# Kernel optimization log

Hardware: AMD Instinct MI355X
Metric: run time of the kernel (lower is better)

Reference implementation:

```python
import jax, jax.numpy as jnp
import numpy as np

HEADS = 16
D_HEAD = 64
EPS = 1e-5


def _ln(x, g, b):
    m = jnp.mean(x, axis=-1, keepdims=True)
    v = jnp.var(x, axis=-1, keepdims=True)
    return (x - m) * jax.lax.rsqrt(v + EPS) * g + b


def _attn(xq, xc, Wq, Wk, Wv, Wo, bo):
    # Wq: [dim, inner], Wk/Wv: [ctx_dim, inner], Wo: [inner, dim]
    B, N, _ = xq.shape
    S = xc.shape[1]
    q = (xq @ Wq).reshape(B, N, HEADS, D_HEAD)
    k = (xc @ Wk).reshape(B, S, HEADS, D_HEAD)
    v = (xc @ Wv).reshape(B, S, HEADS, D_HEAD)
    scale = D_HEAD ** -0.5
    scores = jnp.einsum('bnhd,bshd->bhns', q, k) * scale
    attn = jax.nn.softmax(scores, axis=-1)
    out = jnp.einsum('bhns,bshd->bnhd', attn, v).reshape(B, N, HEADS * D_HEAD)
    return out @ Wo + bo


def _geglu_ff(x, Wp, bp, Wf, bf):
    h = x @ Wp + bp  # [B,N,2*inner]
    a, gate = jnp.split(h, 2, axis=-1)
    # torch F.gelu default is exact (erf) gelu
    return (a * jax.nn.gelu(gate, approximate=False)) @ Wf + bf


def setup_inputs() -> dict:
    key = jax.random.key(0)
    ks = jax.random.split(key, 16)
    dim, ctx, inner, ffin = 1024, 768, HEADS * D_HEAD, 4 * 1024
    def w(k, i, o):
        return jax.random.normal(k, (i, o), jnp.float32) * (i ** -0.5)
    inp = {
        'x': jax.random.normal(ks[0], (4, 2048, dim), jnp.float32),
        'context': jax.random.normal(ks[1], (4, 77, ctx), jnp.float32),
        'Wq1': w(ks[2], dim, inner), 'Wk1': w(ks[3], dim, inner), 'Wv1': w(ks[4], dim, inner),
        'Wo1': w(ks[5], inner, dim), 'bo1': jnp.zeros((dim,), jnp.float32),
        'Wq2': w(ks[6], dim, inner), 'Wk2': w(ks[7], ctx, inner), 'Wv2': w(ks[8], ctx, inner),
        'Wo2': w(ks[9], inner, dim), 'bo2': jnp.zeros((dim,), jnp.float32),
        'Wp': w(ks[10], dim, 2 * ffin), 'bp': jnp.zeros((2 * ffin,), jnp.float32),
        'Wf': w(ks[11], ffin, dim), 'bf': jnp.zeros((dim,), jnp.float32),
        'g1': jnp.ones((dim,), jnp.float32), 'b1': jnp.zeros((dim,), jnp.float32),
        'g2': jnp.ones((dim,), jnp.float32), 'b2': jnp.zeros((dim,), jnp.float32),
        'g3': jnp.ones((dim,), jnp.float32), 'b3': jnp.zeros((dim,), jnp.float32),
    }
    return inp


def reference(x, context, Wq1, Wk1, Wv1, Wo1, bo1, Wq2, Wk2, Wv2, Wo2, bo2,
              Wp, bp, Wf, bf, g1, b1, g2, b2, g3, b3):
    x = _attn(_ln(x, g1, b1), _ln(x, g1, b1), Wq1, Wk1, Wv1, Wo1, bo1) + x
    x = _attn(_ln(x, g2, b2), context, Wq2, Wk2, Wv2, Wo2, bo2) + x
    x = _geglu_ff(_ln(x, g3, b3), Wp, bp, Wf, bf) + x
    return x
```

## Files before the change

### kernel.cpp

```cpp
#include <hip/hip_runtime.h>

typedef unsigned short u16;
typedef __bf16 bf16x8 __attribute__((ext_vector_type(8)));
typedef float f32x4 __attribute__((ext_vector_type(4)));

#define HEADS 16
#define DHEAD 64
#define DIM 1024
#define NTOK 2048
#define BATCH 4
#define CTXD 768
#define SCROSS 77
#define FFIN 4096

__device__ inline float bf2f(u16 v) { return __uint_as_float(((unsigned)v) << 16); }
__device__ inline u16 f2bf(float f) {
    unsigned u = __float_as_uint(f);
    unsigned r = u + 0x7fffu + ((u >> 16) & 1u);
    return (u16)(r >> 16);
}
__device__ inline f32x4 f4zero() { f32x4 v; v[0]=0.f; v[1]=0.f; v[2]=0.f; v[3]=0.f; return v; }
__device__ inline bf16x8 as_bf16x8(uint4 u) { union { uint4 a; bf16x8 b; } c; c.a = u; return c.b; }

__device__ inline void gload_lds16(const u16* g, u16* l) {
    __builtin_amdgcn_global_load_lds((const __attribute__((address_space(1))) unsigned*)g,
                                     (__attribute__((address_space(3))) unsigned*)l, 16, 0, 0);
}

__global__ __launch_bounds__(256) void wt_k(const float* __restrict__ W, u16* __restrict__ WT,
                                            int K, int N, float scale, int remap) {
    __shared__ u16 Ts[64][72];
    int k0 = blockIdx.x * 64, n0 = blockIdx.y * 64;
    int t = threadIdx.x;
    int r = t >> 2, c4 = (t & 3) * 16;
    const float* wp = W + (size_t)(k0 + r) * N + n0 + c4;
    #pragma unroll
    for (int j = 0; j < 4; j++) {
        float4 v = *(const float4*)(wp + j * 4);
        Ts[c4 + j * 4 + 0][r] = f2bf(v.x * scale);
        Ts[c4 + j * 4 + 1][r] = f2bf(v.y * scale);
        Ts[c4 + j * 4 + 2][r] = f2bf(v.z * scale);
        Ts[c4 + j * 4 + 3][r] = f2bf(v.w * scale);
    }
    __syncthreads();
    int n = t >> 2, kc = (t & 3) * 16;
    int ng = n0 + n;
    if (remap) ng = ((ng & 4095) >> 4) * 32 + ((ng >> 12) << 4) + (ng & 15);
    u16* op = WT + (size_t)ng * K + k0 + kc;
    *(uint4*)op       = *(const uint4*)&Ts[n][kc];
    *(uint4*)(op + 8) = *(const uint4*)&Ts[n][kc + 8];
}

__global__ __launch_bounds__(256) void cvt_k(const float* __restrict__ X, u16* __restrict__ Y, int n4) {
    int i = blockIdx.x * 256 + threadIdx.x;
    if (i < n4) {
        float4 v = *(const float4*)(X + (size_t)i * 4);
        uint2 o;
        o.x = (unsigned)f2bf(v.x) | ((unsigned)f2bf(v.y) << 16);
        o.y = (unsigned)f2bf(v.z) | ((unsigned)f2bf(v.w) << 16);
        *(uint2*)(Y + (size_t)i * 4) = o;
    }
}

__global__ __launch_bounds__(256) void ln_k(const float* __restrict__ X, const float* __restrict__ G,
                                            const float* __restrict__ Bt, u16* __restrict__ Y) {
    int row = blockIdx.x;
    int t = threadIdx.x;
    int w = t >> 6, lane = t & 63;
    float4 xv = *(const float4*)(X + (size_t)row * DIM + t * 4);
    float s = xv.x + xv.y + xv.z + xv.w;
    float s2 = xv.x*xv.x + xv.y*xv.y + xv.z*xv.z + xv.w*xv.w;
    for (int off = 1; off < 64; off <<= 1) {
        s  += __shfl_xor(s,  off, 64);
        s2 += __shfl_xor(s2, off, 64);
    }
    __shared__ float rs[4], rs2[4];
    if (lane == 0) { rs[w] = s; rs2[w] = s2; }
    __syncthreads();
    float S_ = rs[0] + rs[1] + rs[2] + rs[3];
    float S2_ = rs2[0] + rs2[1] + rs2[2] + rs2[3];
    float mean = S_ * (1.0f / DIM);
    float var = fmaxf(S2_ * (1.0f / DIM) - mean * mean, 0.f);
    float rstd = rsqrtf(var + 1e-5f);
    int col = t * 4;
    float4 g = *(const float4*)(G + col);
    float4 b = *(const float4*)(Bt + col);
    float y0 = (xv.x - mean) * rstd * g.x + b.x;
    float y1 = (xv.y - mean) * rstd * g.y + b.y;
    float y2 = (xv.z - mean) * rstd * g.z + b.z;
    float y3 = (xv.w - mean) * rstd * g.w + b.w;
    uint2 o;
    o.x = (unsigned)f2bf(y0) | ((unsigned)f2bf(y1) << 16);
    o.y = (unsigned)f2bf(y2) | ((unsigned)f2bf(y3) << 16);
    *(uint2*)(Y + (size_t)row * DIM + col) = o;
}

template<typename TC, bool RESID>
__global__ __launch_bounds__(256) void gemm128(const u16* __restrict__ A, int lda,
                                               const u16* __restrict__ BT,
                                               const float* __restrict__ bias, const float* resid,
                                               TC* C, int ldc, int M, int N, int K) {
    __shared__ __align__(16) u16 As[128 * 32];
    __shared__ __align__(16) u16 Bs[128 * 32];
    int m0 = blockIdx.x * 128, n0 = blockIdx.y * 128;
    int t = threadIdx.x;
    int w = t >> 6, lane = t & 63;
    int quad = lane >> 4, l16 = lane & 15;
    int mh = (w & 1) * 64, nh = (w >> 1) * 64;
    f32x4 acc[4][4];
    #pragma unroll
    for (int i = 0; i < 4; i++)
        #pragma unroll
        for (int j = 0; j < 4; j++) acc[i][j] = f4zero();
    int sr = t >> 2;
    int sc8 = (((t & 3) ^ ((sr >> 1) & 3)) * 8);
    int ra0 = min(m0 + sr, M - 1);
    int ra1 = min(m0 + sr + 64, M - 1);
    const u16* ga0 = A + (size_t)ra0 * lda + sc8;
    const u16* ga1 = A + (size_t)ra1 * lda + sc8;
    const u16* gb0 = BT + (size_t)(n0 + sr) * K + sc8;
    const u16* gb1 = BT + (size_t)(n0 + sr + 64) * K + sc8;
    u16* lA0 = &As[w * 512];
    u16* lA1 = &As[2048 + w * 512];
    u16* lB0 = &Bs[w * 512];
    u16* lB1 = &Bs[2048 + w * 512];
    int rq = ((quad ^ ((l16 >> 1) & 3)) * 8);
    for (int k0 = 0; k0 < K; k0 += 32) {
        __syncthreads();
        gload_lds16(ga0 + k0, lA0);
        gload_lds16(ga1 + k0, lA1);
        gload_lds16(gb0 + k0, lB0);
        gload_lds16(gb1 + k0, lB1);
        __syncthreads();
        bf16x8 af[4], bfv[4];
        #pragma unroll
        for (int i = 0; i < 4; i++) {
            af[i]  = as_bf16x8(*(const uint4*)&As[(mh + i * 16 + l16) * 32 + rq]);
            bfv[i] = as_bf16x8(*(const uint4*)&Bs[(nh + i * 16 + l16) * 32 + rq]);
        }
        #pragma unroll
        for (int i = 0; i < 4; i++)
            #pragma unroll
            for (int j = 0; j < 4; j++)
                acc[i][j] = __builtin_amdgcn_mfma_f32_16x16x32_bf16(af[i], bfv[j], acc[i][j], 0, 0, 0);
    }
    #pragma unroll
    for (int j = 0; j < 4; j++) {
        int gn = n0 + nh + j * 16 + l16;
        float bv = bias ? bias[gn] : 0.f;
        #pragma unroll
        for (int i = 0; i < 4; i++) {
            #pragma unroll
            for (int r = 0; r < 4; r++) {
                int gm = m0 + mh + i * 16 + quad * 4 + r;
                if (gm < M) {
                    float v = acc[i][j][r] + bv;
                    if constexpr (RESID) v += resid[(size_t)gm * N + gn];
                    if constexpr (__is_same(TC, u16)) C[(size_t)gm * ldc + gn] = f2bf(v);
                    else                              C[(size_t)gm * ldc + gn] = v;
                }
            }
        }
    }
}


#define BAR() __builtin_amdgcn_s_barrier()
#define SB0() __builtin_amdgcn_sched_barrier(0)
#define PRIO1() __builtin_amdgcn_s_setprio(1)
#define PRIO0() __builtin_amdgcn_s_setprio(0)
#define WAIT_VM6() asm volatile("s_waitcnt vmcnt(6)" ::: "memory")
#define WAIT_VM0() asm volatile("s_waitcnt vmcnt(0)" ::: "memory")
#define WAIT_LGKM0() asm volatile("s_waitcnt lgkmcnt(0)" ::: "memory")
#define WAIT_LGKM8() asm volatile("s_waitcnt lgkmcnt(8)" ::: "memory")

#define STAGE_A_R(P, h, q, TAU) gload_lds16(gA + (size_t)((h) * 128 + (q) * 64) * 1024 + (TAU) * 64, \
                                            lA + (P) * 16384 + (h) * 8192 + (q) * 4096)
#define STAGE_B_R(P, h, q, TAU) gload_lds16(gB + (size_t)((h) * 128 + (q) * 64) * 1024 + (TAU) * 64, \
                                            lB + (P) * 16384 + (h) * 8192 + (q) * 4096)
#define RD_A(P, fi, ks) as_bf16x8(*(const uint4*)(rdA + (P) * 32768 + (fi) * 2048 + ((ks) ? o1 : o0)))
#define RD_B(P, fj, ks) as_bf16x8(*(const uint4*)(rdB + (P) * 32768 + (fj) * 2048 + ((ks) ? o1 : o0)))
#define MM(ai, aj, av, bv) acc[ai][aj] = __builtin_amdgcn_mfma_f32_16x16x32_bf16(av, bv, acc[ai][aj], 0, 0, 0)

#define TILE256(P, S0, S1, T, LAST) do {                                              \
    if (LAST) { WAIT_VM0(); } else { WAIT_VM6(); }                                    \
    BAR(); SB0();                                                                     \
                        \
    Ar[0][0] = RD_A(P, 0, 0); Ar[0][1] = RD_A(P, 0, 1);                               \
    Ar[1][0] = RD_A(P, 1, 0); Ar[1][1] = RD_A(P, 1, 1);                               \
    Ar[2][0] = RD_A(P, 2, 0); Ar[2][1] = RD_A(P, 2, 1);                               \
    Ar[3][0] = RD_A(P, 3, 0); Ar[3][1] = RD_A(P, 3, 1);                               \
    BrA[0][0] = RD_B(P, 0, 0); BrA[0][1] = RD_B(P, 0, 1);                             \
    BrA[1][0] = RD_B(P, 1, 0); BrA[1][1] = RD_B(P, 1, 1);                             \
    if (S0) { STAGE_B_R((P) ^ 1, 1, 0, (T) + 1); STAGE_B_R((P) ^ 1, 1, 1, (T) + 1); } \
    WAIT_LGKM8();                                                                     \
    BAR(); WAIT_LGKM0(); SB0(); PRIO1();                                              \
    MM(0,0,Ar[0][0],BrA[0][0]); MM(1,0,Ar[1][0],BrA[0][0]); MM(2,0,Ar[2][0],BrA[0][0]); MM(3,0,Ar[3][0],BrA[0][0]); \
    MM(0,1,Ar[0][0],BrA[1][0]); MM(1,1,Ar[1][0],BrA[1][0]); MM(2,1,Ar[2][0],BrA[1][0]); MM(3,1,Ar[3][0],BrA[1][0]); \
    MM(0,0,Ar[0][1],BrA[0][1]); MM(1,0,Ar[1][1],BrA[0][1]); MM(2,0,Ar[2][1],BrA[0][1]); MM(3,0,Ar[3][1],BrA[0][1]); \
    MM(0,1,Ar[0][1],BrA[1][1]); MM(1,1,Ar[1][1],BrA[1][1]); MM(2,1,Ar[2][1],BrA[1][1]); MM(3,1,Ar[3][1],BrA[1][1]); \
    PRIO0(); SB0(); BAR();                                                            \
                                       \
    BrB[0][0] = RD_B(P, 2, 0); BrB[0][1] = RD_B(P, 2, 1);                             \
    BrB[1][0] = RD_B(P, 3, 0); BrB[1][1] = RD_B(P, 3, 1);                             \
    if (S1) { STAGE_A_R(P, 0, 0, (T) + 2); STAGE_A_R(P, 1, 0, (T) + 2); }             \
    BAR(); WAIT_LGKM0(); SB0(); PRIO1();                                              \
    MM(0,2,Ar[0][0],BrB[0][0]); MM(1,2,Ar[1][0],BrB[0][0]); MM(2,2,Ar[2][0],BrB[0][0]); MM(3,2,Ar[3][0],BrB[0][0]); \
    MM(0,3,Ar[0][0],BrB[1][0]); MM(1,3,Ar[1][0],BrB[1][0]); MM(2,3,Ar[2][0],BrB[1][0]); MM(3,3,Ar[3][0],BrB[1][0]); \
    MM(0,2,Ar[0][1],BrB[0][1]); MM(1,2,Ar[1][1],BrB[0][1]); MM(2,2,Ar[2][1],BrB[0][1]); MM(3,2,Ar[3][1],BrB[0][1]); \
    MM(0,3,Ar[0][1],BrB[1][1]); MM(1,3,Ar[1][1],BrB[1][1]); MM(2,3,Ar[2][1],BrB[1][1]); MM(3,3,Ar[3][1],BrB[1][1]); \
    PRIO0(); SB0(); BAR();                                                            \
      \
    Ar[0][0] = RD_A(P, 4, 0); Ar[0][1] = RD_A(P, 4, 1);                               \
    Ar[1][0] = RD_A(P, 5, 0); Ar[1][1] = RD_A(P, 5, 1);                               \
    Ar[2][0] = RD_A(P, 6, 0); Ar[2][1] = RD_A(P, 6, 1);                               \
    Ar[3][0] = RD_A(P, 7, 0); Ar[3][1] = RD_A(P, 7, 1);                               \
    if (S1) { STAGE_B_R(P, 0, 0, (T) + 2); STAGE_B_R(P, 0, 1, (T) + 2); }             \
    BAR(); WAIT_LGKM0(); SB0(); PRIO1();                                              \
    MM(4,2,Ar[0][0],BrB[0][0]); MM(5,2,Ar[1][0],BrB[0][0]); MM(6,2,Ar[2][0],BrB[0][0]); MM(7,2,Ar[3][0],BrB[0][0]); \
    MM(4,3,Ar[0][0],BrB[1][0]); MM(5,3,Ar[1][0],BrB[1][0]); MM(6,3,Ar[2][0],BrB[1][0]); MM(7,3,Ar[3][0],BrB[1][0]); \
    MM(4,2,Ar[0][1],BrB[0][1]); MM(5,2,Ar[1][1],BrB[0][1]); MM(6,2,Ar[2][1],BrB[0][1]); MM(7,2,Ar[3][1],BrB[0][1]); \
    MM(4,3,Ar[0][1],BrB[1][1]); MM(5,3,Ar[1][1],BrB[1][1]); MM(6,3,Ar[2][1],BrB[1][1]); MM(7,3,Ar[3][1],BrB[1][1]); \
    PRIO0(); SB0(); BAR();                                                            \
           \
    if (S1) { STAGE_A_R(P, 0, 1, (T) + 2); STAGE_A_R(P, 1, 1, (T) + 2); }             \
    BAR(); SB0(); PRIO1();                                                            \
    MM(4,0,Ar[0][0],BrA[0][0]); MM(5,0,Ar[1][0],BrA[0][0]); MM(6,0,Ar[2][0],BrA[0][0]); MM(7,0,Ar[3][0],BrA[0][0]); \
    MM(4,1,Ar[0][0],BrA[1][0]); MM(5,1,Ar[1][0],BrA[1][0]); MM(6,1,Ar[2][0],BrA[1][0]); MM(7,1,Ar[3][0],BrA[1][0]); \
    MM(4,0,Ar[0][1],BrA[0][1]); MM(5,0,Ar[1][1],BrA[0][1]); MM(6,0,Ar[2][1],BrA[0][1]); MM(7,0,Ar[3][1],BrA[0][1]); \
    MM(4,1,Ar[0][1],BrA[1][1]); MM(5,1,Ar[1][1],BrA[1][1]); MM(6,1,Ar[2][1],BrA[1][1]); MM(7,1,Ar[3][1],BrA[1][1]); \
    PRIO0(); SB0();                                                                   \
} while (0)

template<int NBY, int LDC, int EPI>
__global__ __launch_bounds__(512, 2) void gemm256(const u16* __restrict__ A,
                                                  const u16* __restrict__ BT,
                                                  const float* __restrict__ bias,
                                                  u16* __restrict__ C) {
    __shared__ __align__(16) u16 As[2][16384];
    __shared__ __align__(16) u16 Bs[2][16384];
    int t = threadIdx.x;
    int w = t >> 6, lane = t & 63;
    int quad = lane >> 4, l16 = lane & 15;
    int wm = w >> 2, wn = w & 3;
    int bid = blockIdx.x;
    int cpx = (int)gridDim.x >> 3;
    int swz = (bid & 7) * cpx + (bid >> 3);
    int bx = swz / NBY, by = swz % NBY;
    int m0 = bx << 8, n0 = by << 8;

    int ar = t >> 3;
    int ac = (((t & 7) ^ (ar & 7)) << 3);
    const u16* gA = A + (size_t)(m0 + ar) * 1024 + ac;
    const u16* gB = BT + (size_t)(n0 + ar) * 1024 + ac;
    u16* lA = &As[0][0] + (w << 9);
    u16* lB = &Bs[0][0] + (w << 9);
    const char* rdA = (const char*)&As[0][0] + (((wm << 7) + l16) << 7);
    const char* rdB = (const char*)&Bs[0][0] + (((wn << 6) + l16) << 7);
    int o0 = (quad << 4) ^ ((l16 & 7) << 4);
    int o1 = o0 ^ 64;

    f32x4 acc[8][4];
    #pragma unroll
    for (int i = 0; i < 8; i++)
        #pragma unroll
        for (int j = 0; j < 4; j++) acc[i][j] = f4zero();

    STAGE_A_R(0, 0, 0, 0); STAGE_A_R(0, 1, 0, 0);
    STAGE_B_R(0, 0, 0, 0); STAGE_B_R(0, 0, 1, 0);
    STAGE_A_R(0, 0, 1, 0); STAGE_A_R(0, 1, 1, 0);
    STAGE_B_R(0, 1, 0, 0); STAGE_B_R(0, 1, 1, 0);
    STAGE_A_R(1, 0, 0, 1); STAGE_A_R(1, 1, 0, 1);
    STAGE_B_R(1, 0, 0, 1); STAGE_B_R(1, 0, 1, 1);
    STAGE_A_R(1, 0, 1, 1); STAGE_A_R(1, 1, 1, 1);

    bf16x8 Ar[4][2], BrA[2][2], BrB[2][2];
    #pragma unroll 1
    for (int tt = 0; tt < 14; tt += 2) {
        TILE256(0, 1, 1, tt, 0);
        TILE256(1, 1, 1, tt + 1, 0);
    }
    TILE256(0, 1, 0, 14, 0);
    TILE256(1, 0, 0, 15, 1);

    if constexpr (EPI == 0) {
        int gm0 = m0 + wm * 128 + quad * 4;
        int gn0 = n0 + wn * 64 + l16;
        #pragma unroll
        for (int fi = 0; fi < 8; fi++)
            #pragma unroll
            for (int fj = 0; fj < 4; fj++)
                #pragma unroll
                for (int r = 0; r < 4; r++)
                    C[(size_t)(gm0 + fi * 16 + r) * LDC + gn0 + fj * 16] = f2bf(acc[fi][fj][r]);
    } else {
        int gm0 = m0 + wm * 128 + quad * 4;
        int oc0 = (n0 >> 1) + wn * 32 + l16;
        #pragma unroll
        for (int jp = 0; jp < 2; jp++) {
            int oc = oc0 + jp * 16;
            float ba = bias[oc];
            float bg = bias[FFIN + oc];
            #pragma unroll
            for (int fi = 0; fi < 8; fi++)
                #pragma unroll
                for (int r = 0; r < 4; r++) {
                    float a = acc[fi][2 * jp][r] + ba;
                    float g = acc[fi][2 * jp + 1][r] + bg;
                    float v = a * (0.5f * g * (1.f + erff(g * 0.70710678118654752f)));
                    C[(size_t)(gm0 + fi * 16 + r) * LDC + oc] = f2bf(v);
                }
        }
    }
}

__global__ __launch_bounds__(256) void attn_k(const u16* Q, int ldq, const u16* __restrict__ K,
                                              const u16* __restrict__ V, int ldkv,
                                              u16* O, int S) {
    __shared__ __align__(16) u16 Ksh[128 * 64];
    __shared__ __align__(16) u16 Vt[64 * 128];
    __shared__ __align__(16) u16 Pb[4][16 * 128];
    int bh = blockIdx.x;
    int b = bh >> 4, h = bh & 15;
    int q0 = blockIdx.y * 64;
    int t = threadIdx.x;
    int w = t >> 6, lane = t & 63;
    int quad = lane >> 4, l16 = lane & 15;
    int sw = (l16 & 7) << 3;
    const u16* Qp = Q + ((size_t)b * NTOK + q0) * ldq + h * DHEAD;
    const u16* Kp = K + (size_t)b * S * ldkv + h * DHEAD;
    const u16* Vp = V + (size_t)b * S * ldkv + h * DHEAD;
    bf16x8 qf[2];
    #pragma unroll
    for (int ds = 0; ds < 2; ds++)
        qf[ds] = as_bf16x8(*(const uint4*)(Qp + (size_t)(w * 16 + l16) * ldq + ds * 32 + quad * 8));
    float l_l = 0.f;
    f32x4 o_acc[4];
    #pragma unroll
    for (int dt = 0; dt < 4; dt++) o_acc[dt] = f4zero();
    int kr8 = lane >> 3;
    int ksl = ((lane & 7) ^ kr8) * 8;
    int vd = (t >> 5) * 8;
    int vk = (t & 31) * 4;
    int nkt = (S + 127) / 128;
    for (int kt = 0; kt < nkt; kt++) {
        int kbase = kt * 128;
        bool full = (kbase + 128) <= S;
        __syncthreads();
        #pragma unroll
        for (int i = 0; i < 4; i++) {
            int r = min(kbase + (i * 4 + w) * 8 + kr8, S - 1);
            gload_lds16(Kp + (size_t)r * ldkv + ksl, &Ksh[(i * 4 + w) * 512]);
        }
        {
            union { uint4 u; u16 e[8]; } vr[4];
            #pragma unroll
            for (int j = 0; j < 4; j++) {
                int key = min(kbase + vk + j, S - 1);
                vr[j].u = *(const uint4*)(Vp + (size_t)key * ldkv + vd);
            }
            #pragma unroll
            for (int d = 0; d < 8; d++) {
                int row = vd + d;
                uint2 p;
                p.x = (unsigned)vr[0].e[d] | ((unsigned)vr[1].e[d] << 16);
                p.y = (unsigned)vr[2].e[d] | ((unsigned)vr[3].e[d] << 16);
                *(uint2*)&Vt[row * 128 + (vk ^ ((row & 7) << 3))] = p;
            }
        }
        __syncthreads();
        f32x4 sc[8];
        PRIO1();
        #pragma unroll
        for (int sub = 0; sub < 8; sub++) {
            const u16* kr = &Ksh[(sub * 16 + l16) * 64];
            bf16x8 kf0 = as_bf16x8(*(const uint4*)(kr + ((quad * 8) ^ sw)));
            bf16x8 kf1 = as_bf16x8(*(const uint4*)(kr + ((32 + quad * 8) ^ sw)));
            f32x4 s = __builtin_amdgcn_mfma_f32_16x16x32_bf16(kf0, qf[0], f4zero(), 0, 0, 0);
            sc[sub] = __builtin_amdgcn_mfma_f32_16x16x32_bf16(kf1, qf[1], s, 0, 0, 0);
        }
        PRIO0();
        if (!full) {
            #pragma unroll
            for (int sub = 0; sub < 8; sub++)
                #pragma unroll
                for (int r = 0; r < 4; r++)
                    if (kbase + sub * 16 + quad * 4 + r >= S) sc[sub][r] = -1e30f;
        }
        float psum = 0.f;
        #pragma unroll
        for (int sub = 0; sub < 8; sub++) {
            float p0 = __builtin_amdgcn_exp2f(sc[sub][0]);
            float p1 = __builtin_amdgcn_exp2f(sc[sub][1]);
            float p2 = __builtin_amdgcn_exp2f(sc[sub][2]);
            float p3 = __builtin_amdgcn_exp2f(sc[sub][3]);
            psum += (p0 + p1) + (p2 + p3);
            uint2 pk;
            pk.x = __builtin_amdgcn_perm(__float_as_uint(p1), __float_as_uint(p0), 0x07060302);
            pk.y = __builtin_amdgcn_perm(__float_as_uint(p3), __float_as_uint(p2), 0x07060302);
            *(uint2*)&Pb[w][l16 * 128 + ((sub * 16 + quad * 4) ^ sw)] = pk;
        }
        l_l += psum;
        PRIO1();
        #pragma unroll
        for (int kk = 0; kk < 4; kk++) {
            bf16x8 pf = as_bf16x8(*(const uint4*)&Pb[w][l16 * 128 + ((kk * 32 + quad * 8) ^ sw)]);
            #pragma unroll
            for (int dt = 0; dt < 4; dt++) {
                bf16x8 vf = as_bf16x8(*(const uint4*)&Vt[(dt * 16 + l16) * 128 + ((kk * 32 + quad * 8) ^ sw)]);
                o_acc[dt] = __builtin_amdgcn_mfma_f32_16x16x32_bf16(pf, vf, o_acc[dt], 0, 0, 0);
            }
        }
        PRIO0();
    }
    float l_tot = l_l;
    l_tot += __shfl_xor(l_tot, 16, 64);
    l_tot += __shfl_xor(l_tot, 32, 64);
    #pragma unroll
    for (int r = 0; r < 4; r++) {
        float lr = __shfl(l_tot, quad * 4 + r, 64);
        float invl = (lr > 0.f) ? (1.f / lr) : 0.f;
        int gq = q0 + w * 16 + quad * 4 + r;
        #pragma unroll
        for (int dt = 0; dt < 4; dt++) {
            O[((size_t)b * NTOK + gq) * ldq + h * DHEAD + dt * 16 + l16] = f2bf(o_acc[dt][r] * invl);
        }
    }
}

extern "C" void kernel_launch(void* const* d_in, const int* in_sizes, int n_in,
                              void* d_out, int out_size, void* d_ws, size_t ws_size,
                              hipStream_t stream) {
    const float* x   = (const float*)d_in[0];
    const float* ctx = (const float*)d_in[1];
    const float* Wq1 = (const float*)d_in[2];
    const float* Wk1 = (const float*)d_in[3];
    const float* Wv1 = (const float*)d_in[4];
    const float* Wo1 = (const float*)d_in[5];
    const float* bo1 = (const float*)d_in[6];
    const float* Wq2 = (const float*)d_in[7];
    const float* Wk2 = (const float*)d_in[8];
    const float* Wv2 = (const float*)d_in[9];
    const float* Wo2 = (const float*)d_in[10];
    const float* bo2 = (const float*)d_in[11];
    const float* Wp  = (const float*)d_in[12];
    const float* bp  = (const float*)d_in[13];
    const float* Wf  = (const float*)d_in[14];
    const float* bfb = (const float*)d_in[15];
    const float* g1  = (const float*)d_in[16];
    const float* b1  = (const float*)d_in[17];
    const float* g2  = (const float*)d_in[18];
    const float* b2  = (const float*)d_in[19];
    const float* g3  = (const float*)d_in[20];
    const float* b3  = (const float*)d_in[21];
    float* out = (float*)d_out;

    const int M = BATCH * NTOK;
    const int Mc = BATCH * SCROSS;
    u16* ws = (u16*)d_ws;
    size_t o = 0;
    u16* WqT1 = ws + o; o += (size_t)DIM * DIM;
    u16* WkT1 = ws + o; o += (size_t)DIM * DIM;
    u16* WvT1 = ws + o; o += (size_t)DIM * DIM;
    u16* WoT1 = ws + o; o += (size_t)DIM * DIM;
    u16* WqT2 = ws + o; o += (size_t)DIM * DIM;
    u16* WoT2 = ws + o; o += (size_t)DIM * DIM;
    u16* WkT2 = ws + o; o += (size_t)DIM * CTXD;
    u16* WvT2 = ws + o; o += (size_t)DIM * CTXD;
    u16* WpT  = ws + o; o += (size_t)(2 * FFIN) * DIM;
    u16* WfT  = ws + o; o += (size_t)DIM * FFIN;
    u16* ctxb = ws + o; o += (size_t)Mc * CTXD;
    u16* KVc  = ws + o; o += (size_t)Mc * 2048;
    u16* P    = ws + o; o += (size_t)M * DIM;
    u16* QKV  = ws + o; o += (size_t)M * 3072;
    u16* reg2 = ws + o; o += (size_t)M * DIM * 2;
    float* X1 = (float*)reg2;
    u16* gb = QKV;

    dim3 blk(256);
    const float qscale = 0.125f * 1.4426950408889634f;

    wt_k<<<dim3(16, 16), blk, 0, stream>>>(Wq1, WqT1, DIM, DIM, qscale, 0);
    wt_k<<<dim3(16, 16), blk, 0, stream>>>(Wk1, WkT1, DIM, DIM, 1.f, 0);
    wt_k<<<dim3(16, 16), blk, 0, stream>>>(Wv1, WvT1, DIM, DIM, 1.f, 0);
    wt_k<<<dim3(16, 16), blk, 0, stream>>>(Wo1, WoT1, DIM, DIM, 1.f, 0);
    wt_k<<<dim3(16, 16), blk, 0, stream>>>(Wq2, WqT2, DIM, DIM, qscale, 0);
    wt_k<<<dim3(16, 16), blk, 0, stream>>>(Wo2, WoT2, DIM, DIM, 1.f, 0);
    wt_k<<<dim3(12, 16), blk, 0, stream>>>(Wk2, WkT2, CTXD, DIM, 1.f, 0);
    wt_k<<<dim3(12, 16), blk, 0, stream>>>(Wv2, WvT2, CTXD, DIM, 1.f, 0);
    wt_k<<<dim3(16, 128), blk, 0, stream>>>(Wp, WpT, DIM, 2 * FFIN, 1.f, 1);
    wt_k<<<dim3(64, 16), blk, 0, stream>>>(Wf, WfT, FFIN, DIM, 1.f, 0);
    cvt_k<<<dim3((Mc * CTXD / 4 + 255) / 256), blk, 0, stream>>>(ctx, ctxb, Mc * CTXD / 4);

    ln_k<<<dim3(M), blk, 0, stream>>>(x, g1, b1, P);
    gemm128<u16, false><<<dim3(M / 128, 3072 / 128), blk, 0, stream>>>(
        P, DIM, WqT1, nullptr, nullptr, QKV, 3072, M, 3072, DIM);
    attn_k<<<dim3(BATCH * HEADS, NTOK / 64), blk, 0, stream>>>(
        QKV, 3072, QKV + 1024, QKV + 2048, 3072, QKV, NTOK);
    gemm128<float, true><<<dim3(M / 128, DIM / 128), blk, 0, stream>>>(
        QKV, 3072, WoT1, bo1, x, X1, DIM, M, DIM, DIM);

    ln_k<<<dim3(M), blk, 0, stream>>>(X1, g2, b2, P);
    gemm128<u16, false><<<dim3(M / 128, DIM / 128), blk, 0, stream>>>(
        P, DIM, WqT2, nullptr, nullptr, QKV, 3072, M, DIM, DIM);
    gemm128<u16, false><<<dim3((Mc + 127) / 128, 2048 / 128), blk, 0, stream>>>(
        ctxb, CTXD, WkT2, nullptr, nullptr, KVc, 2048, Mc, 2048, CTXD);
    attn_k<<<dim3(BATCH * HEADS, NTOK / 64), blk, 0, stream>>>(
        QKV, 3072, KVc, KVc + 1024, 2048, QKV, SCROSS);
    gemm128<float, true><<<dim3(M / 128, DIM / 128), blk, 0, stream>>>(
        QKV, 3072, WoT2, bo2, X1, out, DIM, M, DIM, DIM);

    ln_k<<<dim3(M), blk, 0, stream>>>(out, g3, b3, P);
    gemm256<32, 4096, 1><<<dim3(32 * 32), dim3(512), 0, stream>>>(P, WpT, bp, gb);
    gemm128<float, true><<<dim3(M / 128, DIM / 128), blk, 0, stream>>>(
        gb, FFIN, WfT, bfb, out, out, DIM, M, DIM, FFIN);
}
```

Before: 912.9 us.

## Software-pipeline LDS fragment reads across tiles and use gemm256 for QKV

The 256-tile GEMM inner loop is restructured so the A/B register fragments for the next tile are prefetched from LDS while the current tile's last MFMA quadrants run. This cuts the barrier count per tile from five to two, using separate A0/A1/B0/B1 register sets and prologue loads. The QKV projection of the first attention block now uses this gemm256 kernel instead of gemm128. The change raises register pressure, and the hand-tuned vmcnt/lgkmcnt waits must stay correct across the tail tiles.

```diff
diff --git a/kernel.cpp b/kernel.cpp
--- a/kernel.cpp
+++ b/kernel.cpp
@@ -170,6 +170,7 @@
 #define PRIO1() __builtin_amdgcn_s_setprio(1)
 #define PRIO0() __builtin_amdgcn_s_setprio(0)
 #define WAIT_VM6() asm volatile("s_waitcnt vmcnt(6)" ::: "memory")
+#define WAIT_VM4() asm volatile("s_waitcnt vmcnt(4)" ::: "memory")
 #define WAIT_VM0() asm volatile("s_waitcnt vmcnt(0)" ::: "memory")
 #define WAIT_LGKM0() asm volatile("s_waitcnt lgkmcnt(0)" ::: "memory")
 #define WAIT_LGKM8() asm volatile("s_waitcnt lgkmcnt(8)" ::: "memory")
@@ -182,54 +183,67 @@
 #define RD_B(P, fj, ks) as_bf16x8(*(const uint4*)(rdB + (P) * 32768 + (fj) * 2048 + ((ks) ? o1 : o0)))
 #define MM(ai, aj, av, bv) acc[ai][aj] = __builtin_amdgcn_mfma_f32_16x16x32_bf16(av, bv, acc[ai][aj], 0, 0, 0)
 
-#define TILE256(P, S0, S1, T, LAST) do {                                              \
-    if (LAST) { WAIT_VM0(); } else { WAIT_VM6(); }                                    \
-    BAR(); SB0();                                                                     \
-                        \
-    Ar[0][0] = RD_A(P, 0, 0); Ar[0][1] = RD_A(P, 0, 1);                               \
-    Ar[1][0] = RD_A(P, 1, 0); Ar[1][1] = RD_A(P, 1, 1);                               \
-    Ar[2][0] = RD_A(P, 2, 0); Ar[2][1] = RD_A(P, 2, 1);                               \
-    Ar[3][0] = RD_A(P, 3, 0); Ar[3][1] = RD_A(P, 3, 1);                               \
-    BrA[0][0] = RD_B(P, 0, 0); BrA[0][1] = RD_B(P, 0, 1);                             \
-    BrA[1][0] = RD_B(P, 1, 0); BrA[1][1] = RD_B(P, 1, 1);                             \
+#define Q00() do { \
+    MM(0,0,A0r[0][0],B0r[0][0]); MM(1,0,A0r[1][0],B0r[0][0]); MM(2,0,A0r[2][0],B0r[0][0]); MM(3,0,A0r[3][0],B0r[0][0]); \
+    MM(0,1,A0r[0][0],B0r[1][0]); MM(1,1,A0r[1][0],B0r[1][0]); MM(2,1,A0r[2][0],B0r[1][0]); MM(3,1,A0r[3][0],B0r[1][0]); \
+    MM(0,0,A0r[0][1],B0r[0][1]); MM(1,0,A0r[1][1],B0r[0][1]); MM(2,0,A0r[2][1],B0r[0][1]); MM(3,0,A0r[3][1],B0r[0][1]); \
+    MM(0,1,A0r[0][1],B0r[1][1]); MM(1,1,A0r[1][1],B0r[1][1]); MM(2,1,A0r[2][1],B0r[1][1]); MM(3,1,A0r[3][1],B0r[1][1]); \
+} while (0)
+#define Q01() do { \
+    MM(0,2,A0r[0][0],B1r[0][0]); MM(1,2,A0r[1][0],B1r[0][0]); MM(2,2,A0r[2][0],B1r[0][0]); MM(3,2,A0r[3][0],B1r[0][0]); \
+    MM(0,3,A0r[0][0],B1r[1][0]); MM(1,3,A0r[1][0],B1r[1][0]); MM(2,3,A0r[2][0],B1r[1][0]); MM(3,3,A0r[3][0],B1r[1][0]); \
+    MM(0,2,A0r[0][1],B1r[0][1]); MM(1,2,A0r[1][1],B1r[0][1]); MM(2,2,A0r[2][1],B1r[0][1]); MM(3,2,A0r[3][1],B1r[0][1]); \
+    MM(0,3,A0r[0][1],B1r[1][1]); MM(1,3,A0r[1][1],B1r[1][1]); MM(2,3,A0r[2][1],B1r[1][1]); MM(3,3,A0r[3][1],B1r[1][1]); \
+} while (0)
+#define Q10() do { \
+    MM(4,0,A1r[0][0],B0r[0][0]); MM(5,0,A1r[1][0],B0r[0][0]); MM(6,0,A1r[2][0],B0r[0][0]); MM(7,0,A1r[3][0],B0r[0][0]); \
+    MM(4,1,A1r[0][0],B0r[1][0]); MM(5,1,A1r[1][0],B0r[1][0]); MM(6,1,A1r[2][0],B0r[1][0]); MM(7,1,A1r[3][0],B0r[1][0]); \
+    MM(4,0,A1r[0][1],B0r[0][1]); MM(5,0,A1r[1][1],B0r[0][1]); MM(6,0,A1r[2][1],B0r[0][1]); MM(7,0,A1r[3][1],B0r[0][1]); \
+    MM(4,1,A1r[0][1],B0r[1][1]); MM(5,1,A1r[1][1],B0r[1][1]); MM(6,1,A1r[2][1],B0r[1][1]); MM(7,1,A1r[3][1],B0r[1][1]); \
+} while (0)
+#define Q11() do { \
+    MM(4,2,A1r[0][0],B1r[0][0]); MM(5,2,A1r[1][0],B1r[0][0]); MM(6,2,A1r[2][0],B1r[0][0]); MM(7,2,A1r[3][0],B1r[0][0]); \
+    MM(4,3,A1r[0][0],B1r[1][0]); MM(5,3,A1r[1][0],B1r[1][0]); MM(6,3,A1r[2][0],B1r[1][0]); MM(7,3,A1r[3][0],B1r[1][0]); \
+    MM(4,2,A1r[0][1],B1r[0][1]); MM(5,2,A1r[1][1],B1r[0][1]); MM(6,2,A1r[2][1],B1r[0][1]); MM(7,2,A1r[3][1],B1r[0][1]); \
+    MM(4,3,A1r[0][1],B1r[1][1]); MM(5,3,A1r[1][1],B1r[1][1]); MM(6,3,A1r[2][1],B1r[1][1]); MM(7,3,A1r[3][1],B1r[1][1]); \
+} while (0)
+
+#define TILEX(P, S0, S1, T, MIDW, ENDW, LAST) do {                                    \
+       \
+    B1r[0][0] = RD_B(P, 2, 0); B1r[0][1] = RD_B(P, 2, 1);                             \
+    B1r[1][0] = RD_B(P, 3, 0); B1r[1][1] = RD_B(P, 3, 1);                             \
     if (S0) { STAGE_B_R((P) ^ 1, 1, 0, (T) + 1); STAGE_B_R((P) ^ 1, 1, 1, (T) + 1); } \
-    WAIT_LGKM8();                                                                     \
-    BAR(); WAIT_LGKM0(); SB0(); PRIO1();                                              \
-    MM(0,0,Ar[0][0],BrA[0][0]); MM(1,0,Ar[1][0],BrA[0][0]); MM(2,0,Ar[2][0],BrA[0][0]); MM(3,0,Ar[3][0],BrA[0][0]); \
-    MM(0,1,Ar[0][0],BrA[1][0]); MM(1,1,Ar[1][0],BrA[1][0]); MM(2,1,Ar[2][0],BrA[1][0]); MM(3,1,Ar[3][0],BrA[1][0]); \
-    MM(0,0,Ar[0][1],BrA[0][1]); MM(1,0,Ar[1][1],BrA[0][1]); MM(2,0,Ar[2][1],BrA[0][1]); MM(3,0,Ar[3][1],BrA[0][1]); \
-    MM(0,1,Ar[0][1],BrA[1][1]); MM(1,1,Ar[1][1],BrA[1][1]); MM(2,1,Ar[2][1],BrA[1][1]); MM(3,1,Ar[3][1],BrA[1][1]); \
-    PRIO0(); SB0(); BAR();                                                            \
-                                       \
-    BrB[0][0] = RD_B(P, 2, 0); BrB[0][1] = RD_B(P, 2, 1);                             \
-    BrB[1][0] = RD_B(P, 3, 0); BrB[1][1] = RD_B(P, 3, 1);                             \
+    SB0(); PRIO1(); Q00(); PRIO0(); SB0();                                            \
+                 \
+    A1r[0][0] = RD_A(P, 4, 0); A1r[0][1] = RD_A(P, 4, 1);                             \
+    A1r[1][0] = RD_A(P, 5, 0); A1r[1][1] = RD_A(P, 5, 1);                             \
+    A1r[2][0] = RD_A(P, 6, 0); A1r[2][1] = RD_A(P, 6, 1);                             \
+    A1r[3][0] = RD_A(P, 7, 0); A1r[3][1] = RD_A(P, 7, 1);                             \
     if (S1) { STAGE_A_R(P, 0, 0, (T) + 2); STAGE_A_R(P, 1, 0, (T) + 2); }             \
-    BAR(); WAIT_LGKM0(); SB0(); PRIO1();                                              \
-    MM(0,2,Ar[0][0],BrB[0][0]); MM(1,2,Ar[1][0],BrB[0][0]); MM(2,2,Ar[2][0],BrB[0][0]); MM(3,2,Ar[3][0],BrB[0][0]); \
-    MM(0,3,Ar[0][0],BrB[1][0]); MM(1,3,Ar[1][0],BrB[1][0]); MM(2,3,Ar[2][0],BrB[1][0]); MM(3,3,Ar[3][0],BrB[1][0]); \
-    MM(0,2,Ar[0][1],BrB[0][1]); MM(1,2,Ar[1][1],BrB[0][1]); MM(2,2,Ar[2][1],BrB[0][1]); MM(3,2,Ar[3][1],BrB[0][1]); \
-    MM(0,3,Ar[0][1],BrB[1][1]); MM(1,3,Ar[1][1],BrB[1][1]); MM(2,3,Ar[2][1],BrB[1][1]); MM(3,3,Ar[3][1],BrB[1][1]); \
-    PRIO0(); SB0(); BAR();                                                            \
-      \
-    Ar[0][0] = RD_A(P, 4, 0); Ar[0][1] = RD_A(P, 4, 1);                               \
-    Ar[1][0] = RD_A(P, 5, 0); Ar[1][1] = RD_A(P, 5, 1);                               \
-    Ar[2][0] = RD_A(P, 6, 0); Ar[2][1] = RD_A(P, 6, 1);                               \
-    Ar[3][0] = RD_A(P, 7, 0); Ar[3][1] = RD_A(P, 7, 1);                               \
+    WAIT_LGKM8(); SB0(); PRIO1(); Q01(); PRIO0(); SB0();                              \
+        \
+    WAIT_LGKM0();                                                                     \
+    if (!(LAST)) { MIDW; BAR(); }                                                     \
+    SB0();                                                                            \
+                \
+    if (!(LAST)) {                                                                    \
+        A0r[0][0] = RD_A((P) ^ 1, 0, 0); A0r[0][1] = RD_A((P) ^ 1, 0, 1);             \
+        A0r[1][0] = RD_A((P) ^ 1, 1, 0); A0r[1][1] = RD_A((P) ^ 1, 1, 1);             \
+        A0r[2][0] = RD_A((P) ^ 1, 2, 0); A0r[2][1] = RD_A((P) ^ 1, 2, 1);             \
+        A0r[3][0] = RD_A((P) ^ 1, 3, 0); A0r[3][1] = RD_A((P) ^ 1, 3, 1);             \
+    }                                                                                 \
     if (S1) { STAGE_B_R(P, 0, 0, (T) + 2); STAGE_B_R(P, 0, 1, (T) + 2); }             \
-    BAR(); WAIT_LGKM0(); SB0(); PRIO1();                                              \
-    MM(4,2,Ar[0][0],BrB[0][0]); MM(5,2,Ar[1][0],BrB[0][0]); MM(6,2,Ar[2][0],BrB[0][0]); MM(7,2,Ar[3][0],BrB[0][0]); \
-    MM(4,3,Ar[0][0],BrB[1][0]); MM(5,3,Ar[1][0],BrB[1][0]); MM(6,3,Ar[2][0],BrB[1][0]); MM(7,3,Ar[3][0],BrB[1][0]); \
-    MM(4,2,Ar[0][1],BrB[0][1]); MM(5,2,Ar[1][1],BrB[0][1]); MM(6,2,Ar[2][1],BrB[0][1]); MM(7,2,Ar[3][1],BrB[0][1]); \
-    MM(4,3,Ar[0][1],BrB[1][1]); MM(5,3,Ar[1][1],BrB[1][1]); MM(6,3,Ar[2][1],BrB[1][1]); MM(7,3,Ar[3][1],BrB[1][1]); \
-    PRIO0(); SB0(); BAR();                                                            \
-           \
+    SB0(); PRIO1(); Q10(); PRIO0(); SB0();                                            \
+                                \
+    if (!(LAST)) {                                                                    \
+        B0r[0][0] = RD_B((P) ^ 1, 0, 0); B0r[0][1] = RD_B((P) ^ 1, 0, 1);             \
+        B0r[1][0] = RD_B((P) ^ 1, 1, 0); B0r[1][1] = RD_B((P) ^ 1, 1, 1);             \
+    }                                                                                 \
+       \
     if (S1) { STAGE_A_R(P, 0, 1, (T) + 2); STAGE_A_R(P, 1, 1, (T) + 2); }             \
-    BAR(); SB0(); PRIO1();                                                            \
-    MM(4,0,Ar[0][0],BrA[0][0]); MM(5,0,Ar[1][0],BrA[0][0]); MM(6,0,Ar[2][0],BrA[0][0]); MM(7,0,Ar[3][0],BrA[0][0]); \
-    MM(4,1,Ar[0][0],BrA[1][0]); MM(5,1,Ar[1][0],BrA[1][0]); MM(6,1,Ar[2][0],BrA[1][0]); MM(7,1,Ar[3][0],BrA[1][0]); \
-    MM(4,0,Ar[0][1],BrA[0][1]); MM(5,0,Ar[1][1],BrA[0][1]); MM(6,0,Ar[2][1],BrA[0][1]); MM(7,0,Ar[3][1],BrA[0][1]); \
-    MM(4,1,Ar[0][1],BrA[1][1]); MM(5,1,Ar[1][1],BrA[1][1]); MM(6,1,Ar[2][1],BrA[1][1]); MM(7,1,Ar[3][1],BrA[1][1]); \
-    PRIO0(); SB0();                                                                   \
+    SB0(); PRIO1(); Q11(); PRIO0(); SB0();                                            \
+    if (!(LAST)) { WAIT_LGKM0(); ENDW; BAR(); }                                       \
+    SB0();                                                                            \
 } while (0)
 
 template<int NBY, int LDC, int EPI>
@@ -273,15 +287,25 @@
     STAGE_A_R(1, 0, 0, 1); STAGE_A_R(1, 1, 0, 1);
     STAGE_B_R(1, 0, 0, 1); STAGE_B_R(1, 0, 1, 1);
     STAGE_A_R(1, 0, 1, 1); STAGE_A_R(1, 1, 1, 1);
-
-    bf16x8 Ar[4][2], BrA[2][2], BrB[2][2];
+    WAIT_VM6();
+    BAR();
+    bf16x8 A0r[4][2], A1r[4][2], B0r[2][2], B1r[2][2];
+    A0r[0][0] = RD_A(0, 0, 0); A0r[0][1] = RD_A(0, 0, 1);
+    A0r[1][0] = RD_A(0, 1, 0); A0r[1][1] = RD_A(0, 1, 1);
+    A0r[2][0] = RD_A(0, 2, 0); A0r[2][1] = RD_A(0, 2, 1);
+    A0r[3][0] = RD_A(0, 3, 0); A0r[3][1] = RD_A(0, 3, 1);
+    B0r[0][0] = RD_B(0, 0, 0); B0r[0][1] = RD_B(0, 0, 1);
+    B0r[1][0] = RD_B(0, 1, 0); B0r[1][1] = RD_B(0, 1, 1);
+    WAIT_LGKM0();
+    BAR();
+
     #pragma unroll 1
     for (int tt = 0; tt < 14; tt += 2) {
-        TILE256(0, 1, 1, tt, 0);
-        TILE256(1, 1, 1, tt + 1, 0);
-    }
-    TILE256(0, 1, 0, 14, 0);
-    TILE256(1, 0, 0, 15, 1);
+        TILEX(0, 1, 1, tt,     WAIT_VM6(), WAIT_VM6(), 0);
+        TILEX(1, 1, 1, tt + 1, WAIT_VM6(), WAIT_VM6(), 0);
+    }
+    TILEX(0, 1, 0, 14, WAIT_VM4(), WAIT_VM0(), 0);
+    TILEX(1, 0, 0, 15, (void)0, (void)0, 1);
 
     if constexpr (EPI == 0) {
         int gm0 = m0 + wm * 128 + quad * 4;
@@ -493,8 +517,7 @@
     cvt_k<<<dim3((Mc * CTXD / 4 + 255) / 256), blk, 0, stream>>>(ctx, ctxb, Mc * CTXD / 4);
 
     ln_k<<<dim3(M), blk, 0, stream>>>(x, g1, b1, P);
-    gemm128<u16, false><<<dim3(M / 128, 3072 / 128), blk, 0, stream>>>(
-        P, DIM, WqT1, nullptr, nullptr, QKV, 3072, M, 3072, DIM);
+    gemm256<12, 3072, 0><<<dim3(32 * 12), dim3(512), 0, stream>>>(P, WqT1, nullptr, QKV);
     attn_k<<<dim3(BATCH * HEADS, NTOK / 64), blk, 0, stream>>>(
         QKV, 3072, QKV + 1024, QKV + 2048, 3072, QKV, NTOK);
     gemm128<float, true><<<dim3(M / 128, DIM / 128), blk, 0, stream>>>(
```

Measured after the change: 873.9 us. 1.04x faster.
